# Optimization experiments

Hardware: AMD Instinct MI355X
Metric: run time of the kernel (lower is better)

The kernel has to match this reference:

```python
import jax, jax.numpy as jnp
import numpy as np

N = 50000
NEG_SLOPE = 0.2  # PyG GATConv default leaky_relu slope


def _gat_layer(x, src, dst, W, a_s, a_d, b):
    # x: [N, Fin]; W: [Fin, H*C]; a_s, a_d: [H, C]; b: [C]
    H, C = a_s.shape
    xp = (x @ W).reshape(N, H, C)                      # projected node features per head
    alpha_s = jnp.einsum('nhc,hc->nh', xp, a_s)        # [N, H]
    alpha_d = jnp.einsum('nhc,hc->nh', xp, a_d)        # [N, H]
    e = jax.nn.leaky_relu(alpha_s[src] + alpha_d[dst], NEG_SLOPE)  # [E, H]
    # segment softmax over incoming edges of each dst node
    m = jax.ops.segment_max(e, dst, num_segments=N)
    m = jnp.where(jnp.isfinite(m), m, 0.0)
    p = jnp.exp(e - jax.lax.stop_gradient(m)[dst])
    denom = jax.ops.segment_sum(p, dst, num_segments=N)
    alpha = p / denom[dst]                             # [E, H]
    # scatter-aggregate messages
    out = jax.ops.segment_sum(alpha[:, :, None] * xp[src], dst, num_segments=N)  # [N, H, C]
    return out.mean(axis=1) + b                        # concat=False -> mean over heads


def setup_inputs() -> dict:
    key = jax.random.key(0)
    ks = jax.random.split(key, 16)
    IN, HID, OUT, H = 128, 64, 40, 4
    E = 800000
    x = jax.random.normal(ks[0], (N, IN), dtype=jnp.float32)
    edge_index = jax.random.randint(ks[1], (2, E), 0, N, dtype=jnp.int64)

    def mk(kw, ka, fin, fout):
        s = 1.0 / np.sqrt(fin)
        W = jax.random.normal(kw, (fin, H * fout), dtype=jnp.float32) * s
        a_s = jax.random.normal(ka, (H, fout), dtype=jnp.float32) * 0.1
        a_d = jax.random.normal(jax.random.fold_in(ka, 1), (H, fout), dtype=jnp.float32) * 0.1
        b = jnp.zeros((fout,), dtype=jnp.float32)
        return W, a_s, a_d, b

    W1, as1, ad1, b1 = mk(ks[2], ks[3], IN, HID)
    W2, as2, ad2, b2 = mk(ks[4], ks[5], HID, HID)
    W3, as3, ad3, b3 = mk(ks[6], ks[7], HID, OUT)
    return dict(x=x, edge_index=edge_index,
                W1=W1, as1=as1, ad1=ad1, b1=b1,
                W2=W2, as2=as2, ad2=ad2, b2=b2,
                W3=W3, as3=as3, ad3=ad3, b3=b3)


def reference(x, edge_index, W1, as1, ad1, b1, W2, as2, ad2, b2, W3, as3, ad3, b3):
    # PyG GATConv adds self-loops by default
    loop = jnp.arange(N, dtype=edge_index.dtype)
    src = jnp.concatenate([edge_index[0], loop])
    dst = jnp.concatenate([edge_index[1], loop])
    h = jax.nn.relu(_gat_layer(x, src, dst, W1, as1, ad1, b1))   # dropout is identity in eval
    h = jax.nn.relu(_gat_layer(h, src, dst, W2, as2, ad2, b2))
    h = jax.nn.relu(_gat_layer(h, src, dst, W3, as3, ad3, b3))
    return jax.nn.log_softmax(h, axis=-1)
```

## Files before the change

kernel.cpp:

```cpp
#include <hip/hip_runtime.h>
#include <math.h>

#define NNODES 50000
#define NEG_SLOPE 0.2f

typedef unsigned short ushort8v __attribute__((ext_vector_type(8)));
typedef unsigned short ushort4v __attribute__((ext_vector_type(4)));
typedef short short8v __attribute__((ext_vector_type(8)));
typedef float f32x4 __attribute__((ext_vector_type(4)));
typedef float f32x2 __attribute__((ext_vector_type(2)));

__device__ __forceinline__ unsigned short f2bf(float f){
    unsigned u = __float_as_uint(f);
    u += 0x7fff + ((u >> 16) & 1);
    return (unsigned short)(u >> 16);
}

__device__ __forceinline__ void emit_wa(const float* __restrict__ W, const float* __restrict__ a_s,
                                        const float* __restrict__ a_d, unsigned short* __restrict__ Wt,
                                        int Kin, int C, int id){
    const int n = id / Kin, k = id - n * Kin;
    float v = 0.f;
    if(n < 8){
        const int hh = n & 3;
        const float* av = (n < 4) ? a_s : a_d;
        for(int c = 0; c < C; c++) v += W[(size_t)k * (4 * C) + hh * C + c] * av[hh * C + c];
    }
    Wt[id] = f2bf(v);
}

__device__ __forceinline__ void emit_wc(const float* __restrict__ W, unsigned short* __restrict__ Wt,
                                        int Kin, int C, int id){
    const int c = id / (4 * Kin);
    const int hk = id - c * (4 * Kin);
    const int h = hk / Kin, k = hk - h * Kin;
    const float v = (c < C) ? W[(size_t)k * (4 * C) + h * C + c] * 0.25f : 0.f;
    Wt[id] = f2bf(v);
}

__global__ void initprep_kernel(const unsigned long long* __restrict__ e, int* __restrict__ flag,
                                int* __restrict__ deg, int N,
                                const float* __restrict__ x, unsigned short* __restrict__ xbf, int X4,
                                const float* __restrict__ W1, const float* __restrict__ as1, const float* __restrict__ ad1,
                                const float* __restrict__ W2, const float* __restrict__ as2, const float* __restrict__ ad2,
                                const float* __restrict__ W3, const float* __restrict__ as3, const float* __restrict__ ad3,
                                unsigned short* __restrict__ Wa1, unsigned short* __restrict__ Wa2,
                                unsigned short* __restrict__ Wa3, unsigned short* __restrict__ Wc1,
                                unsigned short* __restrict__ Wc2, unsigned short* __restrict__ Wc3){
    if(blockIdx.x == 0 && threadIdx.x < 64){
        const unsigned long long v = e[threadIdx.x];
        const unsigned long long mask = __ballot(v >= (1ULL << 32));
        if(threadIdx.x == 0) *flag = (mask == 0ULL) ? 1 : 0;
    }
    int id = blockIdx.x * blockDim.x + threadIdx.x;
    if(id < N) deg[id] = 0;
    if(id < X4){
        const float4 v = *(const float4*)&x[(size_t)id * 4];
        ushort4v o;
        o[0] = f2bf(v.x); o[1] = f2bf(v.y); o[2] = f2bf(v.z); o[3] = f2bf(v.w);
        *(ushort4v*)&xbf[(size_t)id * 4] = o;
        return;
    }
    id -= X4;
    if(id < 16 * 128){ emit_wa(W1, as1, ad1, Wa1, 128, 64, id); return; }
    id -= 16 * 128;
    if(id < 16 * 64){ emit_wa(W2, as2, ad2, Wa2, 64, 64, id); return; }
    id -= 16 * 64;
    if(id < 16 * 64){ emit_wa(W3, as3, ad3, Wa3, 64, 40, id); return; }
    id -= 16 * 64;
    if(id < 64 * 512){ emit_wc(W1, Wc1, 128, 64, id); return; }
    id -= 64 * 512;
    if(id < 64 * 256){ emit_wc(W2, Wc2, 64, 64, id); return; }
    id -= 64 * 256;
    if(id < 48 * 256){ emit_wc(W3, Wc3, 64, 40, id); }
}

__global__ void hist_kernel(const void* __restrict__ e, const int* __restrict__ flag,
                            int* __restrict__ deg, int E){
    const int i = blockIdx.x * blockDim.x + threadIdx.x;
    if(i < E){
        const int d = (*flag) ? (int)((const long long*)e)[E + i] : ((const int*)e)[E + i];
        atomicAdd(&deg[d], 1);
    }
}

__global__ __launch_bounds__(512) void scan1_kernel(const int* __restrict__ deg,
                                                    int* __restrict__ excl,
                                                    int* __restrict__ bsum, int n){
    __shared__ int sh[512];
    const int t = threadIdx.x;
    const int gid = blockIdx.x * 512 + t;
    const int v = (gid < n) ? deg[gid] : 0;
    sh[t] = v;
    __syncthreads();
    for(int off = 1; off < 512; off <<= 1){
        const int add = (t >= off) ? sh[t - off] : 0;
        __syncthreads();
        sh[t] += add;
        __syncthreads();
    }
    if(gid < n) excl[gid] = sh[t] - v;
    if(t == 511) bsum[blockIdx.x] = sh[511];
}

__global__ __launch_bounds__(128) void scan2_kernel(int* __restrict__ bsum, int nb){
    __shared__ int sh[128];
    const int t = threadIdx.x;
    const int v = (t < nb) ? bsum[t] : 0;
    sh[t] = v;
    __syncthreads();
    for(int off = 1; off < 128; off <<= 1){
        const int add = (t >= off) ? sh[t - off] : 0;
        __syncthreads();
        sh[t] += add;
        __syncthreads();
    }
    if(t < nb) bsum[t] = sh[t] - v;
}

__global__ void scan3_kernel(const int* __restrict__ excl, const int* __restrict__ bsum,
                             int* __restrict__ row_ptr, int* __restrict__ cursor,
                             int n, int E){
    const int gid = blockIdx.x * blockDim.x + threadIdx.x;
    if(gid < n){
        const int r = excl[gid] + bsum[gid >> 9];
        row_ptr[gid] = r;
        cursor[gid] = r;
    }
    if(gid == 0) row_ptr[n] = E;
}

__global__ void scatter_kernel(const void* __restrict__ e, const int* __restrict__ flag,
                               int* __restrict__ cursor, int* __restrict__ col, int E){
    const int i = blockIdx.x * blockDim.x + threadIdx.x;
    if(i < E){
        int s, d;
        if(*flag){ s = (int)((const long long*)e)[i]; d = (int)((const long long*)e)[E + i]; }
        else     { s = ((const int*)e)[i];            d = ((const int*)e)[E + i]; }
        const int pos = atomicAdd(&cursor[d], 1);
        col[pos] = s;
    }
}

template<int K>
__global__ __launch_bounds__(256) void agemm_kernel(const unsigned short* __restrict__ A,
                                                    const unsigned short* __restrict__ Wa,
                                                    float* __restrict__ ea, float* __restrict__ ed,
                                                    int M){
    const int lane = threadIdx.x & 63;
    const int wave = threadIdx.x >> 6;
    const int quad = lane >> 4;
    const int l16 = lane & 15;
    const int bm = blockIdx.x * 64;
    const int m = min(bm + wave * 16 + l16, M - 1);
    f32x4 acc = {0,0,0,0};
    #pragma unroll
    for(int k0 = 0; k0 < K; k0 += 32){
        const short8v a = *(const short8v*)&A[(size_t)m * K + k0 + quad * 8];
        const short8v b = *(const short8v*)&Wa[(size_t)l16 * K + k0 + quad * 8];
        acc = __builtin_amdgcn_mfma_f32_16x16x32_bf16(a, b, acc, 0, 0, 0);
    }
    if(l16 < 8){
        const int h = l16 & 3;
        float* dst = (l16 < 4) ? ea : ed;
        const int rbase = bm + wave * 16 + quad * 4;
        #pragma unroll
        for(int r = 0; r < 4; r++){
            const int row = rbase + r;
            if(row < M){
                const float v = acc[r];
                *(f32x2*)&dst[(size_t)row * 8 + 2 * h] = (f32x2){__expf(v), __expf(NEG_SLOPE * v)};
            }
        }
    }
}

template<int K>
__global__ __launch_bounds__(256) void gather_kernel(const unsigned short* __restrict__ X,
                                                     const int* __restrict__ row_ptr,
                                                     const int* __restrict__ col,
                                                     const float* __restrict__ ea,
                                                     const float* __restrict__ ed,
                                                     unsigned short* __restrict__ g){
    constexpr int CPL = K / 16;
    constexpr int PAIRS = CPL / 2;
    const int lane = threadIdx.x & 63;
    const int wave = threadIdx.x >> 6;
    const int n = blockIdx.x * 4 + wave;
    const int slot = lane >> 4;
    const int pos = lane & 15;
    const int rs = row_ptr[n], re = row_ptr[n + 1];
    const int T = re - rs + 1;
    const float4 edA = *(const float4*)&ed[(size_t)n * 8];
    const float4 edB = *(const float4*)&ed[(size_t)n * 8 + 4];

    f32x2 acc[4][PAIRS];
    #pragma unroll
    for(int h = 0; h < 4; h++)
        #pragma unroll
        for(int p = 0; p < PAIRS; p++) acc[h][p] = (f32x2){0.f, 0.f};
    float dnm[4] = {0.f, 0.f, 0.f, 0.f};

    auto body = [&](int e){
        const int s = (e < re) ? col[e] : n;
        const float4 eaA = *(const float4*)&ea[(size_t)s * 8];
        const float4 eaB = *(const float4*)&ea[(size_t)s * 8 + 4];
        const float w0 = fmaxf(eaA.x * edA.x, eaA.y * edA.y);
        const float w1 = fmaxf(eaA.z * edA.z, eaA.w * edA.w);
        const float w2 = fmaxf(eaB.x * edB.x, eaB.y * edB.y);
        const float w3 = fmaxf(eaB.z * edB.z, eaB.w * edB.w);
        dnm[0] += w0; dnm[1] += w1; dnm[2] += w2; dnm[3] += w3;
        unsigned u[PAIRS];
        if constexpr(PAIRS == 2){
            const uint2 t2 = *(const uint2*)&X[(size_t)s * K + pos * CPL];
            u[0] = t2.x; u[1] = t2.y;
        } else {
            const uint4 t4 = *(const uint4*)&X[(size_t)s * K + pos * CPL];
            u[0] = t4.x; u[1] = t4.y; u[2] = t4.z; u[3] = t4.w;
        }
        #pragma unroll
        for(int p = 0; p < PAIRS; p++){
            const f32x2 v = {__uint_as_float(u[p] << 16), __uint_as_float(u[p] & 0xffff0000u)};
            acc[0][p] += (f32x2){w0, w0} * v;
            acc[1][p] += (f32x2){w1, w1} * v;
            acc[2][p] += (f32x2){w2, w2} * v;
            acc[3][p] += (f32x2){w3, w3} * v;
        }
    };

    int k = 0;
    for(; k + 8 <= T; k += 8){ body(rs + k + slot); body(rs + k + 4 + slot); }
    for(; k + 4 <= T; k += 4){ body(rs + k + slot); }
    if(k < T && slot < T - k){ body(rs + k + slot); }

    #pragma unroll
    for(int msk = 16; msk < 64; msk <<= 1){
        #pragma unroll
        for(int h = 0; h < 4; h++){
            #pragma unroll
            for(int p = 0; p < PAIRS; p++){
                acc[h][p][0] += __shfl_xor(acc[h][p][0], msk);
                acc[h][p][1] += __shfl_xor(acc[h][p][1], msk);
            }
            dnm[h] += __shfl_xor(dnm[h], msk);
        }
    }
    if(lane < 16){
        #pragma unroll
        for(int h = 0; h < 4; h++){
            const float sc = 1.f / dnm[h];
            if constexpr(PAIRS == 2){
                ushort4v o;
                o[0] = f2bf(acc[h][0][0] * sc); o[1] = f2bf(acc[h][0][1] * sc);
                o[2] = f2bf(acc[h][1][0] * sc); o[3] = f2bf(acc[h][1][1] * sc);
                *(ushort4v*)&g[(size_t)n * (4 * K) + h * K + pos * CPL] = o;
            } else {
                ushort8v o;
                #pragma unroll
                for(int p = 0; p < 4; p++){
                    o[2*p]   = f2bf(acc[h][p][0] * sc);
                    o[2*p+1] = f2bf(acc[h][p][1] * sc);
                }
                *(ushort8v*)&g[(size_t)n * (4 * K) + h * K + pos * CPL] = o;
            }
        }
    }
}

template<int KC, int NC, bool FINAL, bool ALPHA>
__global__ __launch_bounds__(256) void pgemm_kernel(const unsigned short* __restrict__ A,
                                                    const unsigned short* __restrict__ Bt,
                                                    const float* __restrict__ bias,
                                                    void* __restrict__ outv,
                                                    const unsigned short* __restrict__ Wa,
                                                    float* __restrict__ ea,
                                                    float* __restrict__ ed,
                                                    int M){
    constexpr int NT = (NC + 15) / 16;
    __shared__ unsigned short lh[ALPHA ? 4 : 1][16][72];
    const int lane = threadIdx.x & 63;
    const int wave = threadIdx.x >> 6;
    const int quad = lane >> 4;
    const int l16 = lane & 15;
    const int bm = blockIdx.x * 64;
    const int m = min(bm + wave * 16 + l16, M - 1);
    const size_t arow = (size_t)m * KC;

    f32x4 acc[NT];
    #pragma unroll
    for(int t = 0; t < NT; t++) acc[t] = (f32x4){0,0,0,0};

    for(int k0 = 0; k0 < KC; k0 += 32){
        const short8v a = *(const short8v*)&A[arow + k0 + quad * 8];
        #pragma unroll
        for(int t = 0; t < NT; t++){
            const short8v b = *(const short8v*)&Bt[(size_t)(t * 16 + l16) * KC + k0 + quad * 8];
            acc[t] = __builtin_amdgcn_mfma_f32_16x16x32_bf16(a, b, acc[t], 0, 0, 0);
        }
    }
    const int rbase = bm + wave * 16 + quad * 4;
    if(!FINAL){
        unsigned short* out = (unsigned short*)outv;
        #pragma unroll
        for(int t = 0; t < NT; t++){
            const int c = t * 16 + l16;
            #pragma unroll
            for(int r = 0; r < 4; r++){
                const unsigned short hb = f2bf(fmaxf(acc[t][r] + bias[c], 0.f));
                const int row = rbase + r;
                if(row < M) out[(size_t)row * NC + c] = hb;
                if constexpr(ALPHA) lh[wave][quad * 4 + r][c] = hb;
            }
        }
        if constexpr(ALPHA){
            f32x4 a4 = {0, 0, 0, 0};
            #pragma unroll
            for(int k0 = 0; k0 < 64; k0 += 32){
                const short8v a = *(const short8v*)&lh[wave][l16][k0 + quad * 8];
                const short8v b = *(const short8v*)&Wa[(size_t)l16 * 64 + k0 + quad * 8];
                a4 = __builtin_amdgcn_mfma_f32_16x16x32_bf16(a, b, a4, 0, 0, 0);
            }
            if(l16 < 8){
                const int h = l16 & 3;
                float* dst = (l16 < 4) ? ea : ed;
                #pragma unroll
                for(int r = 0; r < 4; r++){
                    const int row = rbase + r;
                    if(row < M){
                        const float v = a4[r];
                        *(f32x2*)&dst[(size_t)row * 8 + 2 * h] = (f32x2){__expf(v), __expf(NEG_SLOPE * v)};
                    }
                }
            }
        }
    } else {
        float* out = (float*)outv;
        float o[NT][4];
        #pragma unroll
        for(int t = 0; t < NT; t++){
            const int c = t * 16 + l16;
            const bool valid = c < 40;
            const float bc = valid ? bias[c] : 0.f;
            #pragma unroll
            for(int r = 0; r < 4; r++)
                o[t][r] = valid ? fmaxf(acc[t][r] + bc, 0.f) : -INFINITY;
        }
        #pragma unroll
        for(int r = 0; r < 4; r++){
            float mx = o[0][r];
            #pragma unroll
            for(int t = 1; t < NT; t++) mx = fmaxf(mx, o[t][r]);
            #pragma unroll
            for(int off = 1; off < 16; off <<= 1) mx = fmaxf(mx, __shfl_xor(mx, off));
            float se = 0.f;
            #pragma unroll
            for(int t = 0; t < NT; t++) se += (o[t][r] > -INFINITY) ? __expf(o[t][r] - mx) : 0.f;
            #pragma unroll
            for(int off = 1; off < 16; off <<= 1) se += __shfl_xor(se, off);
            const float lz = mx + logf(se);
            const int row = rbase + r;
            if(row < M){
                #pragma unroll
                for(int t = 0; t < NT; t++){
                    const int c = t * 16 + l16;
                    if(c < 40) out[(size_t)row * 40 + c] = o[t][r] - lz;
                }
            }
        }
    }
}

extern "C" void kernel_launch(void* const* d_in, const int* in_sizes, int n_in,
                              void* d_out, int out_size, void* d_ws, size_t ws_size,
                              hipStream_t stream){
    const int N = NNODES;
    const int E = in_sizes[1] / 2;

    const float* x   = (const float*)d_in[0];
    const float* W1  = (const float*)d_in[2];
    const float* as1 = (const float*)d_in[3];
    const float* ad1 = (const float*)d_in[4];
    const float* b1  = (const float*)d_in[5];
    const float* W2  = (const float*)d_in[6];
    const float* as2 = (const float*)d_in[7];
    const float* ad2 = (const float*)d_in[8];
    const float* b2  = (const float*)d_in[9];
    const float* W3  = (const float*)d_in[10];
    const float* as3 = (const float*)d_in[11];
    const float* ad3 = (const float*)d_in[12];
    const float* b3  = (const float*)d_in[13];

    char* ws = (char*)d_ws;
    size_t off = 0;
    auto alloc = [&](size_t bytes) -> void* {
        void* p = ws + off;
        off = (off + bytes + 255) & ~(size_t)255;
        return p;
    };
    int*   flag    = (int*)  alloc(4);
    int*   row_ptr = (int*)  alloc((size_t)(N + 1) * 4);
    int*   colv    = (int*)  alloc((size_t)E * 4);
    int*   cursor  = (int*)  alloc((size_t)N * 4);
    int*   deg     = (int*)  alloc((size_t)N * 4);
    int*   excl    = (int*)  alloc((size_t)N * 4);
    int*   bsum    = (int*)  alloc(128 * 4);
    unsigned short* xbf = (unsigned short*)alloc((size_t)N * 128 * 2);
    unsigned short* Wa1 = (unsigned short*)alloc(16 * 128 * 2);
    unsigned short* Wa2 = (unsigned short*)alloc(16 * 64 * 2);
    unsigned short* Wa3 = (unsigned short*)alloc(16 * 64 * 2);
    unsigned short* Wc1 = (unsigned short*)alloc((size_t)64 * 512 * 2);
    unsigned short* Wc2 = (unsigned short*)alloc((size_t)64 * 256 * 2);
    unsigned short* Wc3 = (unsigned short*)alloc((size_t)48 * 256 * 2);
    float* eav     = (float*)alloc((size_t)N * 8 * 4);
    float* edv     = (float*)alloc((size_t)N * 8 * 4);
    unsigned short* g   = (unsigned short*)alloc((size_t)N * 512 * 2);
    unsigned short* h1  = (unsigned short*)alloc((size_t)N * 64 * 2);
    unsigned short* h2  = (unsigned short*)alloc((size_t)N * 64 * 2);
    (void)ws_size;

    const void* eraw = d_in[1];

    const int X4 = N * 128 / 4;
    const int prepTotal = X4 + 16*128 + 16*64 + 16*64 + 64*512 + 64*256 + 48*256;
    initprep_kernel<<<(prepTotal + 255) / 256, 256, 0, stream>>>(
        (const unsigned long long*)eraw, flag, deg, N, x, xbf, X4,
        W1, as1, ad1, W2, as2, ad2, W3, as3, ad3,
        Wa1, Wa2, Wa3, Wc1, Wc2, Wc3);

    hist_kernel<<<(E + 255) / 256, 256, 0, stream>>>(eraw, flag, deg, E);
    const int nbScan = (N + 511) / 512;
    scan1_kernel<<<nbScan, 512, 0, stream>>>(deg, excl, bsum, N);
    scan2_kernel<<<1, 128, 0, stream>>>(bsum, nbScan);
    scan3_kernel<<<(N + 255) / 256, 256, 0, stream>>>(excl, bsum, row_ptr, cursor, N, E);
    scatter_kernel<<<(E + 255) / 256, 256, 0, stream>>>(eraw, flag, cursor, colv, E);

    const int nodeBlocks = N / 4;
    const int mBlocks = (N + 63) / 64;

    agemm_kernel<128><<<mBlocks, 256, 0, stream>>>(xbf, Wa1, eav, edv, N);
    gather_kernel<128><<<nodeBlocks, 256, 0, stream>>>(xbf, row_ptr, colv, eav, edv, g);
    pgemm_kernel<512, 64, false, true><<<mBlocks, 256, 0, stream>>>(g, Wc1, b1, h1, Wa2, eav, edv, N);

    gather_kernel<64><<<nodeBlocks, 256, 0, stream>>>(h1, row_ptr, colv, eav, edv, g);
    pgemm_kernel<256, 64, false, true><<<mBlocks, 256, 0, stream>>>(g, Wc2, b2, h2, Wa3, eav, edv, N);

    gather_kernel<64><<<nodeBlocks, 256, 0, stream>>>(h2, row_ptr, colv, eav, edv, g);
    pgemm_kernel<256, 40, true, false><<<mBlocks, 256, 0, stream>>>(g, Wc3, b3, d_out, nullptr, nullptr, nullptr, N);
}
```

Baseline: 421.9 us.

## Sort destination nodes by degree to balance gather wave workloads

Builds a degree-bucketed permutation of nodes, using a counting sort over degrees clamped to 255 fused into the existing scan kernels. The gather kernels then process nodes in descending-degree order, so waves in the same block get similar edge counts and load imbalance shrinks. The cost is extra atomics during preprocessing, one more indirection per wave, and less locality between node index and output rows. The atomicAdd in scan3 also makes the order within each bucket nondeterministic.

```diff
diff --git a/kernel.cpp b/kernel.cpp
--- a/kernel.cpp
+++ b/kernel.cpp
@@ -39,7 +39,7 @@
 }
 
 __global__ void initprep_kernel(const unsigned long long* __restrict__ e, int* __restrict__ flag,
-                                int* __restrict__ deg, int N,
+                                int* __restrict__ deg, int* __restrict__ bincnt, int N,
                                 const float* __restrict__ x, unsigned short* __restrict__ xbf, int X4,
                                 const float* __restrict__ W1, const float* __restrict__ as1, const float* __restrict__ ad1,
                                 const float* __restrict__ W2, const float* __restrict__ as2, const float* __restrict__ ad2,
@@ -53,6 +53,7 @@
         if(threadIdx.x == 0) *flag = (mask == 0ULL) ? 1 : 0;
     }
     int id = blockIdx.x * blockDim.x + threadIdx.x;
+    if(id < 256) bincnt[id] = 0;
     if(id < N) deg[id] = 0;
     if(id < X4){
         const float4 v = *(const float4*)&x[(size_t)id * 4];
@@ -86,11 +87,13 @@
 
 __global__ __launch_bounds__(512) void scan1_kernel(const int* __restrict__ deg,
                                                     int* __restrict__ excl,
-                                                    int* __restrict__ bsum, int n){
+                                                    int* __restrict__ bsum,
+                                                    int* __restrict__ bincnt, int n){
     __shared__ int sh[512];
     const int t = threadIdx.x;
     const int gid = blockIdx.x * 512 + t;
     const int v = (gid < n) ? deg[gid] : 0;
+    if(gid < n) atomicAdd(&bincnt[min(v, 255)], 1);
     sh[t] = v;
     __syncthreads();
     for(int off = 1; off < 512; off <<= 1){
@@ -103,29 +106,41 @@
     if(t == 511) bsum[blockIdx.x] = sh[511];
 }
 
-__global__ __launch_bounds__(128) void scan2_kernel(int* __restrict__ bsum, int nb){
-    __shared__ int sh[128];
+__global__ __launch_bounds__(256) void scan2_kernel(int* __restrict__ bsum, int nb,
+                                                    int* __restrict__ bincnt,
+                                                    int* __restrict__ bincur){
+    __shared__ int sh[256];
+    __shared__ int sb[256];
     const int t = threadIdx.x;
     const int v = (t < nb) ? bsum[t] : 0;
     sh[t] = v;
+    const int c = bincnt[t];
+    sb[t] = c;
     __syncthreads();
-    for(int off = 1; off < 128; off <<= 1){
-        const int add = (t >= off) ? sh[t - off] : 0;
+    for(int off = 1; off < 256; off <<= 1){
+        const int addA = (t >= off) ? sh[t - off] : 0;
+        const int addB = (t + off < 256) ? sb[t + off] : 0;
         __syncthreads();
-        sh[t] += add;
+        sh[t] += addA;
+        sb[t] += addB;
         __syncthreads();
     }
     if(t < nb) bsum[t] = sh[t] - v;
+    bincur[t] = sb[t] - c;
 }
 
 __global__ void scan3_kernel(const int* __restrict__ excl, const int* __restrict__ bsum,
+                             const int* __restrict__ deg,
                              int* __restrict__ row_ptr, int* __restrict__ cursor,
+                             int* __restrict__ bincur, int* __restrict__ perm,
                              int n, int E){
     const int gid = blockIdx.x * blockDim.x + threadIdx.x;
     if(gid < n){
         const int r = excl[gid] + bsum[gid >> 9];
         row_ptr[gid] = r;
         cursor[gid] = r;
+        const int pos = atomicAdd(&bincur[min(deg[gid], 255)], 1);
+        perm[pos] = gid;
     }
     if(gid == 0) row_ptr[n] = E;
 }
@@ -179,6 +194,7 @@
 __global__ __launch_bounds__(256) void gather_kernel(const unsigned short* __restrict__ X,
                                                      const int* __restrict__ row_ptr,
                                                      const int* __restrict__ col,
+                                                     const int* __restrict__ perm,
                                                      const float* __restrict__ ea,
                                                      const float* __restrict__ ed,
                                                      unsigned short* __restrict__ g){
@@ -186,7 +202,7 @@
     constexpr int PAIRS = CPL / 2;
     const int lane = threadIdx.x & 63;
     const int wave = threadIdx.x >> 6;
-    const int n = blockIdx.x * 4 + wave;
+    const int n = perm[blockIdx.x * 4 + wave];
     const int slot = lane >> 4;
     const int pos = lane & 15;
     const int rs = row_ptr[n], re = row_ptr[n + 1];
@@ -403,7 +419,10 @@
     int*   cursor  = (int*)  alloc((size_t)N * 4);
     int*   deg     = (int*)  alloc((size_t)N * 4);
     int*   excl    = (int*)  alloc((size_t)N * 4);
-    int*   bsum    = (int*)  alloc(128 * 4);
+    int*   bsum    = (int*)  alloc(256 * 4);
+    int*   bincnt  = (int*)  alloc(256 * 4);
+    int*   bincur  = (int*)  alloc(256 * 4);
+    int*   perm    = (int*)  alloc((size_t)N * 4);
     unsigned short* xbf = (unsigned short*)alloc((size_t)N * 128 * 2);
     unsigned short* Wa1 = (unsigned short*)alloc(16 * 128 * 2);
     unsigned short* Wa2 = (unsigned short*)alloc(16 * 64 * 2);
@@ -423,27 +442,28 @@
     const int X4 = N * 128 / 4;
     const int prepTotal = X4 + 16*128 + 16*64 + 16*64 + 64*512 + 64*256 + 48*256;
     initprep_kernel<<<(prepTotal + 255) / 256, 256, 0, stream>>>(
-        (const unsigned long long*)eraw, flag, deg, N, x, xbf, X4,
+        (const unsigned long long*)eraw, flag, deg, bincnt, N, x, xbf, X4,
         W1, as1, ad1, W2, as2, ad2, W3, as3, ad3,
         Wa1, Wa2, Wa3, Wc1, Wc2, Wc3);
 
     hist_kernel<<<(E + 255) / 256, 256, 0, stream>>>(eraw, flag, deg, E);
     const int nbScan = (N + 511) / 512;
-    scan1_kernel<<<nbScan, 512, 0, stream>>>(deg, excl, bsum, N);
-    scan2_kernel<<<1, 128, 0, stream>>>(bsum, nbScan);
-    scan3_kernel<<<(N + 255) / 256, 256, 0, stream>>>(excl, bsum, row_ptr, cursor, N, E);
+    scan1_kernel<<<nbScan, 512, 0, stream>>>(deg, excl, bsum, bincnt, N);
+    scan2_kernel<<<1, 256, 0, stream>>>(bsum, nbScan, bincnt, bincur);
+    scan3_kernel<<<(N + 255) / 256, 256, 0, stream>>>(excl, bsum, deg, row_ptr, cursor,
+                                                      bincur, perm, N, E);
     scatter_kernel<<<(E + 255) / 256, 256, 0, stream>>>(eraw, flag, cursor, colv, E);
 
     const int nodeBlocks = N / 4;
     const int mBlocks = (N + 63) / 64;
 
     agemm_kernel<128><<<mBlocks, 256, 0, stream>>>(xbf, Wa1, eav, edv, N);
-    gather_kernel<128><<<nodeBlocks, 256, 0, stream>>>(xbf, row_ptr, colv, eav, edv, g);
+    gather_kernel<128><<<nodeBlocks, 256, 0, stream>>>(xbf, row_ptr, colv, perm, eav, edv, g);
     pgemm_kernel<512, 64, false, true><<<mBlocks, 256, 0, stream>>>(g, Wc1, b1, h1, Wa2, eav, edv, N);
 
-    gather_kernel<64><<<nodeBlocks, 256, 0, stream>>>(h1, row_ptr, colv, eav, edv, g);
+    gather_kernel<64><<<nodeBlocks, 256, 0, stream>>>(h1, row_ptr, colv, perm, eav, edv, g);
     pgemm_kernel<256, 64, false, true><<<mBlocks, 256, 0, stream>>>(g, Wc2, b2, h2, Wa3, eav, edv, N);
 
-    gather_kernel<64><<<nodeBlocks, 256, 0, stream>>>(h2, row_ptr, colv, eav, edv, g);
+    gather_kernel<64><<<nodeBlocks, 256, 0, stream>>>(h2, row_ptr, colv, perm, eav, edv, g);
     pgemm_kernel<256, 40, true, false><<<mBlocks, 256, 0, stream>>>(g, Wc3, b3, d_out, nullptr, nullptr, nullptr, N);
 }
```

New measurement: 692.6 us. 64.2% more time.
